# Kernel tuning notes

Measured on AMD Instinct MI355X. Metric: run time of the kernel, lower is better.

Reference implementation:

```python
import math
import jax, jax.numpy as jnp
import numpy as np

CHANNELS = 512
OUT_CHANNELS = 512
N_HEADS = 8
K_CHANNELS = CHANNELS // N_HEADS
WINDOW = 4


def _get_relative_embeddings(emb, length):
    # emb: [1, 2*WINDOW+1, d] -> [1, 2*length-1, d]
    max_rel = 2 * WINDOW + 1
    pad_length = max(0, length - (WINDOW + 1))
    start = max(0, WINDOW + 1 - length)
    end = max_rel + 2 * length - 1
    if pad_length > 0:
        emb = jnp.pad(emb, ((0, 0), (pad_length, pad_length), (0, 0)))
    return emb[:, start:end]


def _rel_to_abs(x):
    # x: [b, h, l, 2l-1] -> [b, h, l, l] via skewing trick
    b, h, l, _ = x.shape
    x = jnp.pad(x, ((0, 0), (0, 0), (0, 0), (0, 1)))
    x_flat = x.reshape(b, h, l * 2 * l)
    x_flat = jnp.pad(x_flat, ((0, 0), (0, 0), (0, l - 1)))
    return x_flat.reshape(b, h, l + 1, 2 * l - 1)[..., :l, l - 1:]


def _abs_to_rel(x):
    # x: [b, h, l, l] -> [b, h, l, 2l-1]
    b, h, l, _ = x.shape
    x = jnp.pad(x, ((0, 0), (0, 0), (0, 0), (0, l - 1)))
    x_flat = x.reshape(b, h, -1)
    x_flat = jnp.pad(x_flat, ((0, 0), (0, 0), (l, 0)))
    return x_flat.reshape(b, h, l, 2 * l)[..., 1:]


def setup_inputs() -> dict:
    key = jax.random.key(0)
    ks = jax.random.split(key, 12)
    B, T = 4, 1024
    w_std = 1.0 / math.sqrt(CHANNELS)
    rel_std = K_CHANNELS ** (-0.5)
    return {
        'x': jax.random.normal(ks[0], (B, T, CHANNELS), jnp.float32),
        'c': jax.random.normal(ks[1], (B, T, CHANNELS), jnp.float32),
        'Wq': jax.random.normal(ks[2], (CHANNELS, CHANNELS), jnp.float32) * w_std,
        'bq': jnp.zeros((CHANNELS,), jnp.float32),
        'Wk': jax.random.normal(ks[3], (CHANNELS, CHANNELS), jnp.float32) * w_std,
        'bk': jnp.zeros((CHANNELS,), jnp.float32),
        'Wv': jax.random.normal(ks[4], (CHANNELS, CHANNELS), jnp.float32) * w_std,
        'bv': jnp.zeros((CHANNELS,), jnp.float32),
        'Wo': jax.random.normal(ks[5], (CHANNELS, OUT_CHANNELS), jnp.float32) * w_std,
        'bo': jnp.zeros((OUT_CHANNELS,), jnp.float32),
        'emb_rel_k': jax.random.normal(ks[6], (1, 2 * WINDOW + 1, K_CHANNELS), jnp.float32) * rel_std,
        'emb_rel_v': jax.random.normal(ks[7], (1, 2 * WINDOW + 1, K_CHANNELS), jnp.float32) * rel_std,
    }


def reference(x, c, Wq, bq, Wk, bk, Wv, bv, Wo, bo, emb_rel_k, emb_rel_v):
    b, t_t, _ = x.shape
    t_s = c.shape[1]
    # 1x1 convs == pointwise dense projections
    q = x @ Wq + bq
    k = c @ Wk + bk
    v = c @ Wv + bv
    q = q.reshape(b, t_t, N_HEADS, K_CHANNELS).transpose(0, 2, 1, 3)
    k = k.reshape(b, t_s, N_HEADS, K_CHANNELS).transpose(0, 2, 1, 3)
    v = v.reshape(b, t_s, N_HEADS, K_CHANNELS).transpose(0, 2, 1, 3)
    q_scaled = q / math.sqrt(K_CHANNELS)
    scores = jnp.einsum('bhtd,bhsd->bhts', q_scaled, k)
    # relative position bias via skewing trick (heads_share=True -> rel emb head dim 1)
    rel_k = _get_relative_embeddings(emb_rel_k, t_s)[0]  # [2*t_s-1, d]
    rel_logits = jnp.einsum('bhtd,md->bhtm', q_scaled, rel_k)
    scores = scores + _rel_to_abs(rel_logits)
    p_attn = jax.nn.softmax(scores, axis=-1)
    out = jnp.einsum('bhts,bhsd->bhtd', p_attn, v)
    rel_w = _abs_to_rel(p_attn)  # [b, h, t, 2t-1]
    rel_v = _get_relative_embeddings(emb_rel_v, t_s)[0]  # [2*t_s-1, d]
    out = out + jnp.einsum('bhtm,md->bhtd', rel_w, rel_v)
    out = out.transpose(0, 2, 1, 3).reshape(b, t_t, CHANNELS)
    return out @ Wo + bo
```

## Files before the change

### kernel.cpp

```cpp
#include <hip/hip_runtime.h>
#include <hip/hip_bf16.h>

#define B_ 4
#define T_ 1024
#define C_ 512
#define H_ 8

typedef __attribute__((ext_vector_type(8))) short short8;
typedef __attribute__((ext_vector_type(4))) float floatx4;

__device__ __forceinline__ unsigned short f2bs(float f) {
    __hip_bfloat16 h = __float2bfloat16(f);
    return *(unsigned short*)&h;
}
__device__ __forceinline__ float bs2f(unsigned short u) {
    __hip_bfloat16 h;
    *(unsigned short*)&h = u;
    return __bfloat162float(h);
}

__device__ __forceinline__ void gload_lds16(const void* g, void* l) {
    __builtin_amdgcn_global_load_lds(
        (const __attribute__((address_space(1))) unsigned int*)g,
        (__attribute__((address_space(3))) unsigned int*)l, 16, 0, 0);
}

__global__ __launch_bounds__(256) void prep(
    const float* __restrict__ x, const float* __restrict__ c,
    const float* __restrict__ Wq, const float* __restrict__ Wk,
    const float* __restrict__ Wv, const float* __restrict__ Wo,
    unsigned short* __restrict__ xb, unsigned short* __restrict__ cb,
    unsigned short* __restrict__ WT)
{
    __shared__ unsigned short tileT[32][33];
    const int bx = blockIdx.x, tid = threadIdx.x;
    if (bx < 2048) {
        const float* src = (bx < 1024) ? x : c;
        unsigned short* dst = (bx < 1024) ? xb : cb;
        const size_t base = (size_t)(bx & 1023) * 2048 + (size_t)tid * 8;
        const float4 a = *(const float4*)&src[base];
        const float4 b = *(const float4*)&src[base + 4];
        short8 o;
        o[0] = (short)f2bs(a.x); o[1] = (short)f2bs(a.y);
        o[2] = (short)f2bs(a.z); o[3] = (short)f2bs(a.w);
        o[4] = (short)f2bs(b.x); o[5] = (short)f2bs(b.y);
        o[6] = (short)f2bs(b.z); o[7] = (short)f2bs(b.w);
        *(short8*)&dst[base] = o;
    } else {
        const int r = bx - 2048;
        const int w = r >> 8, tile = r & 255;
        const int k0 = (tile >> 4) * 32, n0 = (tile & 15) * 32;
        const float* W = (w == 0) ? Wq : (w == 1) ? Wk : (w == 2) ? Wv : Wo;
        unsigned short* out = WT + (size_t)w * 512 * 512;
        const int kk = tid >> 3, ns = (tid & 7) * 4;
        const float4 v = *(const float4*)&W[(size_t)(k0 + kk) * 512 + n0 + ns];
        tileT[ns + 0][kk] = f2bs(v.x);
        tileT[ns + 1][kk] = f2bs(v.y);
        tileT[ns + 2][kk] = f2bs(v.z);
        tileT[ns + 3][kk] = f2bs(v.w);
        __syncthreads();
        const int nn = tid >> 3, ks = (tid & 7) * 4;
        ushort4 o;
        o.x = tileT[nn][ks + 0]; o.y = tileT[nn][ks + 1];
        o.z = tileT[nn][ks + 2]; o.w = tileT[nn][ks + 3];
        *(ushort4*)&out[(size_t)(n0 + nn) * 512 + k0 + ks] = o;
    }
}

template <int BROWS>
__device__ __forceinline__ void gemm_stage(
    const unsigned short* __restrict__ A, const unsigned short* __restrict__ Bt,
    int m0, int n0, int k0, int wave, int lrow, int lseg,
    unsigned short* sAb, unsigned short* sBb)
{
    #pragma unroll
    for (int j = 0; j < 2; j++) {
        const int rA = wave * 32 + j * 16 + lrow;
        gload_lds16((const char*)A + ((size_t)(m0 + rA) * 512 + k0) * 2 + lseg,
                    &sAb[(size_t)(wave * 32 + j * 16) * 32]);
    }
    if constexpr (BROWS == 128) {
        #pragma unroll
        for (int j = 0; j < 2; j++) {
            const int rB = wave * 32 + j * 16 + lrow;
            gload_lds16((const char*)Bt + ((size_t)(n0 + rB) * 512 + k0) * 2 + lseg,
                        &sBb[(size_t)(wave * 32 + j * 16) * 32]);
        }
    } else {
        const int rB = wave * 16 + lrow;
        gload_lds16((const char*)Bt + ((size_t)(n0 + rB) * 512 + k0) * 2 + lseg,
                    &sBb[(size_t)(wave * 16) * 32]);
    }
}

template <int NT>
struct GemmAccT { floatx4 acc[4][NT]; int mrow, kgrp, mhalf, noff; };

template <int NT>
__device__ __forceinline__ void gemm_coreT(
    const unsigned short* __restrict__ A, const unsigned short* __restrict__ Bt,
    int m0, int n0, unsigned short* sA, unsigned short* sB, GemmAccT<NT>& g)
{
    constexpr int BROWS = NT * 32;
    const int tid = threadIdx.x;
    const int wave = tid >> 6, lane = tid & 63;
    g.mrow = lane & 15;
    g.kgrp = (lane >> 4) * 8;
    g.mhalf = (wave & 1) * 64;
    g.noff = (wave >> 1) * (NT * 16);
    const int lrow = lane >> 2;
    const int lseg = (lane & 3) * 16;

    #pragma unroll
    for (int i = 0; i < 4; i++)
        #pragma unroll
        for (int j = 0; j < NT; j++)
            g.acc[i][j] = (floatx4){0.f, 0.f, 0.f, 0.f};

    gemm_stage<BROWS>(A, Bt, m0, n0, 0, wave, lrow, lseg, sA, sB);

    for (int ck = 0; ck < 16; ck++) {
        const int buf = ck & 1;
        __syncthreads();
        if (ck < 15)
            gemm_stage<BROWS>(A, Bt, m0, n0, (ck + 1) * 32, wave, lrow, lseg,
                              sA + (size_t)(buf ^ 1) * 128 * 32,
                              sB + (size_t)(buf ^ 1) * BROWS * 32);
        const unsigned short* sAb = sA + (size_t)buf * 128 * 32;
        const unsigned short* sBb = sB + (size_t)buf * BROWS * 32;
        short8 af[4], bfv[NT];
        #pragma unroll
        for (int i = 0; i < 4; i++)
            af[i] = *(const short8*)&sAb[(size_t)(g.mhalf + i * 16 + g.mrow) * 32 + g.kgrp];
        #pragma unroll
        for (int i = 0; i < NT; i++)
            bfv[i] = *(const short8*)&sBb[(size_t)(g.noff + i * 16 + g.mrow) * 32 + g.kgrp];
        #pragma unroll
        for (int mt = 0; mt < 4; mt++)
            #pragma unroll
            for (int nt = 0; nt < NT; nt++)
                g.acc[mt][nt] = __builtin_amdgcn_mfma_f32_16x16x32_bf16(
                    af[mt], bfv[nt], g.acc[mt][nt], 0, 0, 0);
    }
}

__global__ __launch_bounds__(256) void qkv_mfma(
    const unsigned short* __restrict__ xb, const unsigned short* __restrict__ cb,
    const unsigned short* __restrict__ WT,
    const float* __restrict__ bq, const float* __restrict__ bk,
    const float* __restrict__ bv,
    unsigned short* __restrict__ Qc, unsigned short* __restrict__ Kc,
    unsigned short* __restrict__ Vtg)
{
    const int z = blockIdx.z;
    const unsigned short* A  = (z == 0) ? xb : cb;
    const unsigned short* Bt = WT + (size_t)z * 262144;
    const float* bias        = (z == 0) ? bq : (z == 1) ? bk : bv;
    const float scale        = (z == 0) ? 0.125f : 1.0f;

    __shared__ __align__(16) unsigned short sA[2 * 128 * 32];
    __shared__ __align__(16) unsigned short sB[2 * 128 * 32];

    const int m0 = blockIdx.y * 128, n0 = blockIdx.x * 128;
    GemmAccT<4> g;
    gemm_coreT<4>(A, Bt, m0, n0, sA, sB, g);

    const int lane = threadIdx.x & 63;
    const int rowq = (lane >> 4) * 4;
    if (z < 2) {
        unsigned short* Y = (z == 0) ? Qc : Kc;
        #pragma unroll
        for (int nt = 0; nt < 4; nt++) {
            const int n = n0 + g.noff + nt * 16 + g.mrow;
            const float bv_ = bias[n];
            const int h = n >> 6, d = n & 63;
            #pragma unroll
            for (int mt = 0; mt < 4; mt++)
                #pragma unroll
                for (int r = 0; r < 4; r++) {
                    const int m = m0 + g.mhalf + mt * 16 + rowq + r;
                    const int bb = m >> 10, t = m & 1023;
                    Y[(((size_t)bb * H_ + h) * 1024 + t) * 64 + d] =
                        f2bs((g.acc[mt][nt][r] + bv_) * scale);
                }
        }
    } else {
        #pragma unroll
        for (int nt = 0; nt < 4; nt++) {
            const int n = n0 + g.noff + nt * 16 + g.mrow;
            const float bv_ = bias[n];
            const int h = n >> 6, d = n & 63;
            #pragma unroll
            for (int mt = 0; mt < 4; mt++) {
                const int m = m0 + g.mhalf + mt * 16 + rowq;
                const int bb = m >> 10, t = m & 1023;
                ushort4 o4;
                o4.x = f2bs(g.acc[mt][nt][0] + bv_);
                o4.y = f2bs(g.acc[mt][nt][1] + bv_);
                o4.z = f2bs(g.acc[mt][nt][2] + bv_);
                o4.w = f2bs(g.acc[mt][nt][3] + bv_);
                *(ushort4*)&Vtg[(((size_t)bb * H_ + h) * 64 + d) * 1024 + t] = o4;
            }
        }
    }
}

__global__ __launch_bounds__(256) void out_mfma(
    const unsigned short* __restrict__ AOb, const unsigned short* __restrict__ WoT,
    const float* __restrict__ bias, float* __restrict__ out)
{
    __shared__ __align__(16) unsigned short sA[2 * 128 * 32];
    __shared__ __align__(16) unsigned short sB[2 * 64 * 32];

    const int m0 = blockIdx.y * 128, n0 = blockIdx.x * 64;
    GemmAccT<2> g;
    gemm_coreT<2>(AOb, WoT, m0, n0, sA, sB, g);

    const int lane = threadIdx.x & 63;
    const int rowq = (lane >> 4) * 4;
    #pragma unroll
    for (int nt = 0; nt < 2; nt++) {
        const int n = n0 + g.noff + nt * 16 + g.mrow;
        const float bv_ = bias[n];
        #pragma unroll
        for (int mt = 0; mt < 4; mt++)
            #pragma unroll
            for (int r = 0; r < 4; r++) {
                const int m = m0 + g.mhalf + mt * 16 + rowq + r;
                out[(size_t)m * 512 + n] = g.acc[mt][nt][r] + bv_;
            }
    }
}

__device__ __forceinline__ void attn_stage(
    const unsigned short* __restrict__ Kc, const unsigned short* __restrict__ Vtg,
    size_t qkbase, size_t vtbase, int s0, int wave, int ldrow, int gseg,
    unsigned short* KLb, unsigned short* VtLb)
{
    #pragma unroll
    for (int j = 0; j < 2; j++) {
        const int br = wave * 16 + j * 8;
        gload_lds16((const char*)Kc + (qkbase + (size_t)(s0 + br + ldrow) * 64) * 2 + gseg * 16,
                    &KLb[br * 64]);
        gload_lds16((const char*)Vtg + (vtbase + (size_t)(br + ldrow) * 1024 + s0) * 2 + gseg * 16,
                    &VtLb[br * 64]);
    }
}

__global__ __launch_bounds__(256) void attn_mfma(
    const unsigned short* __restrict__ Qc, const unsigned short* __restrict__ Kc,
    const unsigned short* __restrict__ Vtg,
    const float* __restrict__ rk,
    unsigned short* __restrict__ Opart, float* __restrict__ lpart,
    float* __restrict__ bandP)
{
    __shared__ __align__(16) unsigned short KL[2][64 * 64];
    __shared__ __align__(16) unsigned short VtL[2][64 * 64];
    __shared__ __align__(16) unsigned short PL[4][16 * 72];
    __shared__ float qbL[64 * 9];

    const int tb = blockIdx.x, sh = blockIdx.y, bh = blockIdx.z;
    const int tid = threadIdx.x;
    const int wave = tid >> 6, lane = tid & 63;
    const int t0 = tb * 64;
    const int t0w = t0 + wave * 16;
    const size_t qkbase = (size_t)bh * T_ * 64;
    const size_t vtbase = (size_t)bh * 64 * T_;

    const int mrow = lane & 15;
    const int quad = lane >> 4;
    const int kgrp = quad * 8;
    const int x7 = mrow & 7;
    const int ldrow = lane >> 3;
    const int gseg = (lane & 7) ^ ldrow;

    attn_stage(Kc, Vtg, qkbase, vtbase, sh * 512, wave, ldrow, gseg,
               &KL[0][0], &VtL[0][0]);

    for (int idx = tid; idx < 576; idx += 256) {
        const int row = idx / 9, w = idx - row * 9;
        const unsigned short* qp = &Qc[qkbase + (size_t)(t0 + row) * 64];
        float s = 0.f;
        #pragma unroll
        for (int d8 = 0; d8 < 8; d8++) {
            const short8 q8 = *(const short8*)&qp[d8 * 8];
            #pragma unroll
            for (int i = 0; i < 8; i++)
                s = fmaf(bs2f((unsigned short)q8[i]), rk[w * 64 + d8 * 8 + i], s);
        }
        qbL[idx] = s;
    }

    const short8 aQ0 = *(const short8*)&Qc[qkbase + (size_t)(t0w + mrow) * 64 + kgrp];
    const short8 aQ1 = *(const short8*)&Qc[qkbase + (size_t)(t0w + mrow) * 64 + 32 + kgrp];

    floatx4 Oc[4];
    float ls[4] = {0.f, 0.f, 0.f, 0.f};
    #pragma unroll
    for (int dt = 0; dt < 4; dt++) Oc[dt] = (floatx4){0.f, 0.f, 0.f, 0.f};

    unsigned short* Pw = &PL[wave][0];
    float* qbw = &qbL[wave * 16 * 9];

    for (int ck = 0; ck < 8; ck++) {
        const int s0 = sh * 512 + ck * 64;
        const int buf = ck & 1;
        __syncthreads();
        if (ck < 7)
            attn_stage(Kc, Vtg, qkbase, vtbase, s0 + 64, wave, ldrow, gseg,
                       &KL[buf ^ 1][0], &VtL[buf ^ 1][0]);

        floatx4 Sc[4];
        #pragma unroll
        for (int st = 0; st < 4; st++) {
            const int row = st * 16 + mrow;
            const short8 bK0 = *(const short8*)&KL[buf][row * 64 + (quad ^ x7) * 8];
            const short8 bK1 = *(const short8*)&KL[buf][row * 64 + ((4 + quad) ^ x7) * 8];
            floatx4 s4 = {0.f, 0.f, 0.f, 0.f};
            s4 = __builtin_amdgcn_mfma_f32_16x16x32_bf16(aQ0, bK0, s4, 0, 0, 0);
            s4 = __builtin_amdgcn_mfma_f32_16x16x32_bf16(aQ1, bK1, s4, 0, 0, 0);
            Sc[st] = s4;
        }

        #pragma unroll
        for (int st = 0; st < 4; st++) {
            const int diff = s0 + st * 16 - t0w;
            if (diff >= -19 && diff <= 19) {
                #pragma unroll
                for (int r = 0; r < 4; r++) {
                    const int tloc = quad * 4 + r;
                    const int rel = diff + mrow - tloc;
                    float sc = Sc[st][r];
                    const bool inband = (rel >= -4) && (rel <= 4);
                    if (inband) sc += qbw[tloc * 9 + rel + 4];
                    const float p = __expf(sc);
                    if (inband)
                        bandP[((size_t)bh * 1024 + t0w + tloc) * 9 + rel + 4] = p;
                    Pw[tloc * 72 + st * 16 + mrow] = f2bs(p);
                    ls[r] += p;
                }
            } else {
                #pragma unroll
                for (int r = 0; r < 4; r++) {
                    const int tloc = quad * 4 + r;
                    const float p = __expf(Sc[st][r]);
                    Pw[tloc * 72 + st * 16 + mrow] = f2bs(p);
                    ls[r] += p;
                }
            }
        }

        #pragma unroll
        for (int c = 0; c < 2; c++) {
            const short8 aP = *(const short8*)&Pw[mrow * 72 + c * 32 + kgrp];
            #pragma unroll
            for (int dt = 0; dt < 4; dt++) {
                const int segl = (c * 4 + quad) ^ x7;
                const short8 bV = *(const short8*)&VtL[buf][(dt * 16 + mrow) * 64 + segl * 8];
                Oc[dt] = __builtin_amdgcn_mfma_f32_16x16x32_bf16(aP, bV, Oc[dt], 0, 0, 0);
            }
        }
    }

    float lsum[4];
    #pragma unroll
    for (int r = 0; r < 4; r++) {
        float v = ls[r];
        #pragma unroll
        for (int mk = 1; mk < 16; mk <<= 1)
            v += __shfl_xor(v, mk);
        lsum[r] = v;
    }
    if (mrow == 0) {
        #pragma unroll
        for (int r = 0; r < 4; r++)
            lpart[((size_t)sh * 32 + bh) * 1024 + t0w + quad * 4 + r] = lsum[r];
    }

    const size_t ob = (((size_t)sh * 32 + bh) * 1024 + t0w) * 64;
    #pragma unroll
    for (int dt = 0; dt < 4; dt++)
        #pragma unroll
        for (int r = 0; r < 4; r++)
            Opart[ob + (size_t)(quad * 4 + r) * 64 + dt * 16 + mrow] = f2bs(Oc[dt][r]);
}

__global__ __launch_bounds__(256) void combine(
    const unsigned short* __restrict__ Opart, const float* __restrict__ lpart,
    const float* __restrict__ bandP, const float* __restrict__ rv,
    unsigned short* __restrict__ AOb)
{
    const int bh = blockIdx.y;
    const int b = bh >> 3, h = bh & 7;
    const int tid = threadIdx.x;
    const int tr = tid >> 6, d = tid & 63;
    const int t = blockIdx.x * 4 + tr;

    const size_t i0 = ((size_t)bh * 1024 + t) * 64 + d;
    const size_t half = (size_t)32 * 1024 * 64;
    float o = bs2f(Opart[i0]) + bs2f(Opart[half + i0]);
    const float l = lpart[(size_t)bh * 1024 + t] + lpart[(size_t)32 * 1024 + bh * 1024 + t];
    const float inv = 1.f / l;
    o *= inv;
    #pragma unroll
    for (int w = 0; w < 9; w++) {
        const int s = t + w - 4;
        if (s >= 0 && s < 1024)
            o = fmaf(bandP[((size_t)bh * 1024 + t) * 9 + w] * inv, rv[w * 64 + d], o);
    }
    AOb[((size_t)b * 1024 + t) * 512 + h * 64 + d] = f2bs(o);
}

extern "C" void kernel_launch(void* const* d_in, const int* in_sizes, int n_in,
                              void* d_out, int out_size, void* d_ws, size_t ws_size,
                              hipStream_t stream)
{
    const float* x  = (const float*)d_in[0];
    const float* c  = (const float*)d_in[1];
    const float* Wq = (const float*)d_in[2];
    const float* bq = (const float*)d_in[3];
    const float* Wk = (const float*)d_in[4];
    const float* bk = (const float*)d_in[5];
    const float* Wv = (const float*)d_in[6];
    const float* bv = (const float*)d_in[7];
    const float* Wo = (const float*)d_in[8];
    const float* bo = (const float*)d_in[9];
    const float* rk = (const float*)d_in[10];
    const float* rv = (const float*)d_in[11];

    unsigned short* xb  = (unsigned short*)d_ws;
    unsigned short* cb  = xb + (size_t)4096 * 512;
    unsigned short* WT  = cb + (size_t)4096 * 512;
    unsigned short* Qc  = WT + (size_t)4 * 512 * 512;
    unsigned short* Kc  = Qc + (size_t)32 * 1024 * 64;
    unsigned short* Vtg = Kc + (size_t)32 * 1024 * 64;
    unsigned short* AOb = Vtg + (size_t)32 * 1024 * 64;
    float* lpart = (float*)(AOb + (size_t)4096 * 512);
    float* bandP = lpart + (size_t)2 * 32 * 1024;
    unsigned short* Opart = xb;

    prep<<<3072, 256, 0, stream>>>(x, c, Wq, Wk, Wv, Wo, xb, cb, WT);
    qkv_mfma<<<dim3(4, 32, 3), 256, 0, stream>>>(xb, cb, WT, bq, bk, bv, Qc, Kc, Vtg);
    attn_mfma<<<dim3(16, 2, 32), 256, 0, stream>>>(Qc, Kc, Vtg, rk, Opart, lpart, bandP);
    combine<<<dim3(256, 32), 256, 0, stream>>>(Opart, lpart, bandP, rv, AOb);
    out_mfma<<<dim3(8, 32), 256, 0, stream>>>(AOb, WT + (size_t)3 * 262144, bo, (float*)d_out);
}
```

Baseline: 175.9 us.

## Fuse fp32-to-bf16 conversion into QKV GEMM and merge combine into attention

```diff
diff --git a/kernel.cpp b/kernel.cpp
--- a/kernel.cpp
+++ b/kernel.cpp
@@ -26,126 +26,32 @@
 }
 
 __global__ __launch_bounds__(256) void prep(
-    const float* __restrict__ x, const float* __restrict__ c,
     const float* __restrict__ Wq, const float* __restrict__ Wk,
     const float* __restrict__ Wv, const float* __restrict__ Wo,
-    unsigned short* __restrict__ xb, unsigned short* __restrict__ cb,
     unsigned short* __restrict__ WT)
 {
     __shared__ unsigned short tileT[32][33];
-    const int bx = blockIdx.x, tid = threadIdx.x;
-    if (bx < 2048) {
-        const float* src = (bx < 1024) ? x : c;
-        unsigned short* dst = (bx < 1024) ? xb : cb;
-        const size_t base = (size_t)(bx & 1023) * 2048 + (size_t)tid * 8;
-        const float4 a = *(const float4*)&src[base];
-        const float4 b = *(const float4*)&src[base + 4];
-        short8 o;
-        o[0] = (short)f2bs(a.x); o[1] = (short)f2bs(a.y);
-        o[2] = (short)f2bs(a.z); o[3] = (short)f2bs(a.w);
-        o[4] = (short)f2bs(b.x); o[5] = (short)f2bs(b.y);
-        o[6] = (short)f2bs(b.z); o[7] = (short)f2bs(b.w);
-        *(short8*)&dst[base] = o;
-    } else {
-        const int r = bx - 2048;
-        const int w = r >> 8, tile = r & 255;
-        const int k0 = (tile >> 4) * 32, n0 = (tile & 15) * 32;
-        const float* W = (w == 0) ? Wq : (w == 1) ? Wk : (w == 2) ? Wv : Wo;
-        unsigned short* out = WT + (size_t)w * 512 * 512;
-        const int kk = tid >> 3, ns = (tid & 7) * 4;
-        const float4 v = *(const float4*)&W[(size_t)(k0 + kk) * 512 + n0 + ns];
-        tileT[ns + 0][kk] = f2bs(v.x);
-        tileT[ns + 1][kk] = f2bs(v.y);
-        tileT[ns + 2][kk] = f2bs(v.z);
-        tileT[ns + 3][kk] = f2bs(v.w);
-        __syncthreads();
-        const int nn = tid >> 3, ks = (tid & 7) * 4;
-        ushort4 o;
-        o.x = tileT[nn][ks + 0]; o.y = tileT[nn][ks + 1];
-        o.z = tileT[nn][ks + 2]; o.w = tileT[nn][ks + 3];
-        *(ushort4*)&out[(size_t)(n0 + nn) * 512 + k0 + ks] = o;
-    }
-}
-
-template <int BROWS>
-__device__ __forceinline__ void gemm_stage(
-    const unsigned short* __restrict__ A, const unsigned short* __restrict__ Bt,
-    int m0, int n0, int k0, int wave, int lrow, int lseg,
-    unsigned short* sAb, unsigned short* sBb)
-{
-    #pragma unroll
-    for (int j = 0; j < 2; j++) {
-        const int rA = wave * 32 + j * 16 + lrow;
-        gload_lds16((const char*)A + ((size_t)(m0 + rA) * 512 + k0) * 2 + lseg,
-                    &sAb[(size_t)(wave * 32 + j * 16) * 32]);
-    }
-    if constexpr (BROWS == 128) {
-        #pragma unroll
-        for (int j = 0; j < 2; j++) {
-            const int rB = wave * 32 + j * 16 + lrow;
-            gload_lds16((const char*)Bt + ((size_t)(n0 + rB) * 512 + k0) * 2 + lseg,
-                        &sBb[(size_t)(wave * 32 + j * 16) * 32]);
-        }
-    } else {
-        const int rB = wave * 16 + lrow;
-        gload_lds16((const char*)Bt + ((size_t)(n0 + rB) * 512 + k0) * 2 + lseg,
-                    &sBb[(size_t)(wave * 16) * 32]);
-    }
-}
-
-template <int NT>
-struct GemmAccT { floatx4 acc[4][NT]; int mrow, kgrp, mhalf, noff; };
-
-template <int NT>
-__device__ __forceinline__ void gemm_coreT(
-    const unsigned short* __restrict__ A, const unsigned short* __restrict__ Bt,
-    int m0, int n0, unsigned short* sA, unsigned short* sB, GemmAccT<NT>& g)
-{
-    constexpr int BROWS = NT * 32;
-    const int tid = threadIdx.x;
-    const int wave = tid >> 6, lane = tid & 63;
-    g.mrow = lane & 15;
-    g.kgrp = (lane >> 4) * 8;
-    g.mhalf = (wave & 1) * 64;
-    g.noff = (wave >> 1) * (NT * 16);
-    const int lrow = lane >> 2;
-    const int lseg = (lane & 3) * 16;
-
-    #pragma unroll
-    for (int i = 0; i < 4; i++)
-        #pragma unroll
-        for (int j = 0; j < NT; j++)
-            g.acc[i][j] = (floatx4){0.f, 0.f, 0.f, 0.f};
-
-    gemm_stage<BROWS>(A, Bt, m0, n0, 0, wave, lrow, lseg, sA, sB);
-
-    for (int ck = 0; ck < 16; ck++) {
-        const int buf = ck & 1;
-        __syncthreads();
-        if (ck < 15)
-            gemm_stage<BROWS>(A, Bt, m0, n0, (ck + 1) * 32, wave, lrow, lseg,
-                              sA + (size_t)(buf ^ 1) * 128 * 32,
-                              sB + (size_t)(buf ^ 1) * BROWS * 32);
-        const unsigned short* sAb = sA + (size_t)buf * 128 * 32;
-        const unsigned short* sBb = sB + (size_t)buf * BROWS * 32;
-        short8 af[4], bfv[NT];
-        #pragma unroll
-        for (int i = 0; i < 4; i++)
-            af[i] = *(const short8*)&sAb[(size_t)(g.mhalf + i * 16 + g.mrow) * 32 + g.kgrp];
-        #pragma unroll
-        for (int i = 0; i < NT; i++)
-            bfv[i] = *(const short8*)&sBb[(size_t)(g.noff + i * 16 + g.mrow) * 32 + g.kgrp];
-        #pragma unroll
-        for (int mt = 0; mt < 4; mt++)
-            #pragma unroll
-            for (int nt = 0; nt < NT; nt++)
-                g.acc[mt][nt] = __builtin_amdgcn_mfma_f32_16x16x32_bf16(
-                    af[mt], bfv[nt], g.acc[mt][nt], 0, 0, 0);
-    }
+    const int r = blockIdx.x, tid = threadIdx.x;
+    const int w = r >> 8, tile = r & 255;
+    const int k0 = (tile >> 4) * 32, n0 = (tile & 15) * 32;
+    const float* W = (w == 0) ? Wq : (w == 1) ? Wk : (w == 2) ? Wv : Wo;
+    unsigned short* out = WT + (size_t)w * 512 * 512;
+    const int kk = tid >> 3, ns = (tid & 7) * 4;
+    const float4 v = *(const float4*)&W[(size_t)(k0 + kk) * 512 + n0 + ns];
+    tileT[ns + 0][kk] = f2bs(v.x);
+    tileT[ns + 1][kk] = f2bs(v.y);
+    tileT[ns + 2][kk] = f2bs(v.z);
+    tileT[ns + 3][kk] = f2bs(v.w);
+    __syncthreads();
+    const int nn = tid >> 3, ks = (tid & 7) * 4;
+    ushort4 o;
+    o.x = tileT[nn][ks + 0]; o.y = tileT[nn][ks + 1];
+    o.z = tileT[nn][ks + 2]; o.w = tileT[nn][ks + 3];
+    *(ushort4*)&out[(size_t)(n0 + nn) * 512 + k0 + ks] = o;
 }
 
 __global__ __launch_bounds__(256) void qkv_mfma(
-    const unsigned short* __restrict__ xb, const unsigned short* __restrict__ cb,
+    const float* __restrict__ x, const float* __restrict__ cc,
     const unsigned short* __restrict__ WT,
     const float* __restrict__ bq, const float* __restrict__ bk,
     const float* __restrict__ bv,
@@ -153,52 +59,120 @@
     unsigned short* __restrict__ Vtg)
 {
     const int z = blockIdx.z;
-    const unsigned short* A  = (z == 0) ? xb : cb;
+    const float* A32 = (z == 0) ? x : cc;
     const unsigned short* Bt = WT + (size_t)z * 262144;
-    const float* bias        = (z == 0) ? bq : (z == 1) ? bk : bv;
-    const float scale        = (z == 0) ? 0.125f : 1.0f;
+    const float* bias = (z == 0) ? bq : (z == 1) ? bk : bv;
+    const float scale = (z == 0) ? 0.125f : 1.0f;
 
     __shared__ __align__(16) unsigned short sA[2 * 128 * 32];
-    __shared__ __align__(16) unsigned short sB[2 * 128 * 32];
-
-    const int m0 = blockIdx.y * 128, n0 = blockIdx.x * 128;
-    GemmAccT<4> g;
-    gemm_coreT<4>(A, Bt, m0, n0, sA, sB, g);
-
-    const int lane = threadIdx.x & 63;
-    const int rowq = (lane >> 4) * 4;
+    __shared__ __align__(16) unsigned short sB[2 * 64 * 32];
+
+    const int tid = threadIdx.x;
+    const int wave = tid >> 6, lane = tid & 63;
+    const int m0 = blockIdx.y * 128, n0 = blockIdx.x * 64;
+    const int mrow = lane & 15, quad = lane >> 4, kgrp = quad * 8;
+    const int mhalf = (wave & 1) * 64, noff = (wave >> 1) * 32;
+    const int lrow = lane >> 2, lseg = (lane & 3) * 16;
+
+    const int fr0 = tid >> 3;
+    const int fc4 = (tid & 7) * 4;
+
+    floatx4 acc[4][2];
+    #pragma unroll
+    for (int i = 0; i < 4; i++)
+        #pragma unroll
+        for (int j = 0; j < 2; j++)
+            acc[i][j] = (floatx4){0.f, 0.f, 0.f, 0.f};
+
+    float4 a4[4];
+    #pragma unroll
+    for (int p = 0; p < 4; p++)
+        a4[p] = *(const float4*)&A32[(size_t)(m0 + fr0 + p * 32) * 512 + fc4];
+    {
+        const int rB = wave * 16 + lrow;
+        gload_lds16((const char*)Bt + ((size_t)(n0 + rB) * 512) * 2 + lseg,
+                    &sB[(size_t)(wave * 16) * 32]);
+    }
+    #pragma unroll
+    for (int p = 0; p < 4; p++) {
+        ushort4 o;
+        o.x = f2bs(a4[p].x); o.y = f2bs(a4[p].y);
+        o.z = f2bs(a4[p].z); o.w = f2bs(a4[p].w);
+        *(ushort4*)&sA[(fr0 + p * 32) * 32 + fc4] = o;
+    }
+
+    for (int ck = 0; ck < 16; ck++) {
+        const int buf = ck & 1;
+        __syncthreads();
+        if (ck < 15) {
+            const int k0 = (ck + 1) * 32;
+            const int rB = wave * 16 + lrow;
+            gload_lds16((const char*)Bt + ((size_t)(n0 + rB) * 512 + k0) * 2 + lseg,
+                        &sB[(size_t)((buf ^ 1) * 64 + wave * 16) * 32]);
+            #pragma unroll
+            for (int p = 0; p < 4; p++)
+                a4[p] = *(const float4*)&A32[(size_t)(m0 + fr0 + p * 32) * 512 + k0 + fc4];
+        }
+        const unsigned short* sAb = sA + (size_t)buf * 128 * 32;
+        const unsigned short* sBb = sB + (size_t)buf * 64 * 32;
+        short8 af[4], bfv[2];
+        #pragma unroll
+        for (int i = 0; i < 4; i++)
+            af[i] = *(const short8*)&sAb[(size_t)(mhalf + i * 16 + mrow) * 32 + kgrp];
+        #pragma unroll
+        for (int i = 0; i < 2; i++)
+            bfv[i] = *(const short8*)&sBb[(size_t)(noff + i * 16 + mrow) * 32 + kgrp];
+        #pragma unroll
+        for (int mt = 0; mt < 4; mt++)
+            #pragma unroll
+            for (int nt = 0; nt < 2; nt++)
+                acc[mt][nt] = __builtin_amdgcn_mfma_f32_16x16x32_bf16(
+                    af[mt], bfv[nt], acc[mt][nt], 0, 0, 0);
+        if (ck < 15) {
+            unsigned short* dst = sA + (size_t)(buf ^ 1) * 128 * 32;
+            #pragma unroll
+            for (int p = 0; p < 4; p++) {
+                ushort4 o;
+                o.x = f2bs(a4[p].x); o.y = f2bs(a4[p].y);
+                o.z = f2bs(a4[p].z); o.w = f2bs(a4[p].w);
+                *(ushort4*)&dst[(fr0 + p * 32) * 32 + fc4] = o;
+            }
+        }
+    }
+
+    const int rowq = quad * 4;
     if (z < 2) {
         unsigned short* Y = (z == 0) ? Qc : Kc;
         #pragma unroll
-        for (int nt = 0; nt < 4; nt++) {
-            const int n = n0 + g.noff + nt * 16 + g.mrow;
+        for (int nt = 0; nt < 2; nt++) {
+            const int n = n0 + noff + nt * 16 + mrow;
             const float bv_ = bias[n];
             const int h = n >> 6, d = n & 63;
             #pragma unroll
             for (int mt = 0; mt < 4; mt++)
                 #pragma unroll
                 for (int r = 0; r < 4; r++) {
-                    const int m = m0 + g.mhalf + mt * 16 + rowq + r;
+                    const int m = m0 + mhalf + mt * 16 + rowq + r;
                     const int bb = m >> 10, t = m & 1023;
                     Y[(((size_t)bb * H_ + h) * 1024 + t) * 64 + d] =
-                        f2bs((g.acc[mt][nt][r] + bv_) * scale);
+                        f2bs((acc[mt][nt][r] + bv_) * scale);
                 }
         }
     } else {
         #pragma unroll
-        for (int nt = 0; nt < 4; nt++) {
-            const int n = n0 + g.noff + nt * 16 + g.mrow;
+        for (int nt = 0; nt < 2; nt++) {
+            const int n = n0 + noff + nt * 16 + mrow;
             const float bv_ = bias[n];
             const int h = n >> 6, d = n & 63;
             #pragma unroll
             for (int mt = 0; mt < 4; mt++) {
-                const int m = m0 + g.mhalf + mt * 16 + rowq;
+                const int m = m0 + mhalf + mt * 16 + rowq;
                 const int bb = m >> 10, t = m & 1023;
                 ushort4 o4;
-                o4.x = f2bs(g.acc[mt][nt][0] + bv_);
-                o4.y = f2bs(g.acc[mt][nt][1] + bv_);
-                o4.z = f2bs(g.acc[mt][nt][2] + bv_);
-                o4.w = f2bs(g.acc[mt][nt][3] + bv_);
+                o4.x = f2bs(acc[mt][nt][0] + bv_);
+                o4.y = f2bs(acc[mt][nt][1] + bv_);
+                o4.z = f2bs(acc[mt][nt][2] + bv_);
+                o4.w = f2bs(acc[mt][nt][3] + bv_);
                 *(ushort4*)&Vtg[(((size_t)bb * H_ + h) * 64 + d) * 1024 + t] = o4;
             }
         }
@@ -212,22 +186,65 @@
     __shared__ __align__(16) unsigned short sA[2 * 128 * 32];
     __shared__ __align__(16) unsigned short sB[2 * 64 * 32];
 
+    const int tid = threadIdx.x;
+    const int wave = tid >> 6, lane = tid & 63;
     const int m0 = blockIdx.y * 128, n0 = blockIdx.x * 64;
-    GemmAccT<2> g;
-    gemm_coreT<2>(AOb, WoT, m0, n0, sA, sB, g);
-
-    const int lane = threadIdx.x & 63;
-    const int rowq = (lane >> 4) * 4;
+    const int mrow = lane & 15, quad = lane >> 4, kgrp = quad * 8;
+    const int mhalf = (wave & 1) * 64, noff = (wave >> 1) * 32;
+    const int lrow = lane >> 2, lseg = (lane & 3) * 16;
+
+    floatx4 acc[4][2];
+    #pragma unroll
+    for (int i = 0; i < 4; i++)
+        #pragma unroll
+        for (int j = 0; j < 2; j++)
+            acc[i][j] = (floatx4){0.f, 0.f, 0.f, 0.f};
+
+    auto stage = [&](int k0, int bufi) {
+        #pragma unroll
+        for (int j = 0; j < 2; j++) {
+            const int rA = wave * 32 + j * 16 + lrow;
+            gload_lds16((const char*)AOb + ((size_t)(m0 + rA) * 512 + k0) * 2 + lseg,
+                        &sA[(size_t)(bufi * 128 + wave * 32 + j * 16) * 32]);
+        }
+        const int rB = wave * 16 + lrow;
+        gload_lds16((const char*)WoT + ((size_t)(n0 + rB) * 512 + k0) * 2 + lseg,
+                    &sB[(size_t)(bufi * 64 + wave * 16) * 32]);
+    };
+
+    stage(0, 0);
+    for (int ck = 0; ck < 16; ck++) {
+        const int buf = ck & 1;
+        __syncthreads();
+        if (ck < 15) stage((ck + 1) * 32, buf ^ 1);
+        const unsigned short* sAb = sA + (size_t)buf * 128 * 32;
+        const unsigned short* sBb = sB + (size_t)buf * 64 * 32;
+        short8 af[4], bfv[2];
+        #pragma unroll
+        for (int i = 0; i < 4; i++)
+            af[i] = *(const short8*)&sAb[(size_t)(mhalf + i * 16 + mrow) * 32 + kgrp];
+        #pragma unroll
+        for (int i = 0; i < 2; i++)
+            bfv[i] = *(const short8*)&sBb[(size_t)(noff + i * 16 + mrow) * 32 + kgrp];
+        #pragma unroll
+        for (int mt = 0; mt < 4; mt++)
+            #pragma unroll
+            for (int nt = 0; nt < 2; nt++)
+                acc[mt][nt] = __builtin_amdgcn_mfma_f32_16x16x32_bf16(
+                    af[mt], bfv[nt], acc[mt][nt], 0, 0, 0);
+    }
+
+    const int rowq = quad * 4;
     #pragma unroll
     for (int nt = 0; nt < 2; nt++) {
-        const int n = n0 + g.noff + nt * 16 + g.mrow;
+        const int n = n0 + noff + nt * 16 + mrow;
         const float bv_ = bias[n];
         #pragma unroll
         for (int mt = 0; mt < 4; mt++)
             #pragma unroll
             for (int r = 0; r < 4; r++) {
-                const int m = m0 + g.mhalf + mt * 16 + rowq + r;
-                out[(size_t)m * 512 + n] = g.acc[mt][nt][r] + bv_;
+                const int m = m0 + mhalf + mt * 16 + rowq + r;
+                out[(size_t)m * 512 + n] = acc[mt][nt][r] + bv_;
             }
     }
 }
@@ -250,16 +267,19 @@
 __global__ __launch_bounds__(256) void attn_mfma(
     const unsigned short* __restrict__ Qc, const unsigned short* __restrict__ Kc,
     const unsigned short* __restrict__ Vtg,
-    const float* __restrict__ rk,
-    unsigned short* __restrict__ Opart, float* __restrict__ lpart,
-    float* __restrict__ bandP)
+    const float* __restrict__ rk, const float* __restrict__ rv,
+    unsigned short* __restrict__ AOb)
 {
     __shared__ __align__(16) unsigned short KL[2][64 * 64];
     __shared__ __align__(16) unsigned short VtL[2][64 * 64];
     __shared__ __align__(16) unsigned short PL[4][16 * 72];
     __shared__ float qbL[64 * 9];
-
-    const int tb = blockIdx.x, sh = blockIdx.y, bh = blockIdx.z;
+    __shared__ float bandL[64 * 9];
+    __shared__ float rvL[9 * 64];
+    __shared__ float lL[64];
+
+    const int tb = blockIdx.x, bh = blockIdx.y;
+    const int b = bh >> 3, h = bh & 7;
     const int tid = threadIdx.x;
     const int wave = tid >> 6, lane = tid & 63;
     const int t0 = tb * 64;
@@ -274,39 +294,48 @@
     const int ldrow = lane >> 3;
     const int gseg = (lane & 7) ^ ldrow;
 
-    attn_stage(Kc, Vtg, qkbase, vtbase, sh * 512, wave, ldrow, gseg,
-               &KL[0][0], &VtL[0][0]);
+    attn_stage(Kc, Vtg, qkbase, vtbase, 0, wave, ldrow, gseg, &KL[0][0], &VtL[0][0]);
 
     for (int idx = tid; idx < 576; idx += 256) {
+        bandL[idx] = 0.f;
+        rvL[idx] = rv[idx];
         const int row = idx / 9, w = idx - row * 9;
         const unsigned short* qp = &Qc[qkbase + (size_t)(t0 + row) * 64];
-        float s = 0.f;
-        #pragma unroll
-        for (int d8 = 0; d8 < 8; d8++) {
-            const short8 q8 = *(const short8*)&qp[d8 * 8];
-            #pragma unroll
-            for (int i = 0; i < 8; i++)
-                s = fmaf(bs2f((unsigned short)q8[i]), rk[w * 64 + d8 * 8 + i], s);
-        }
-        qbL[idx] = s;
+        float s0a = 0.f, s1a = 0.f, s2a = 0.f, s3a = 0.f;
+        #pragma unroll
+        for (int d8 = 0; d8 < 8; d8 += 4) {
+            const short8 q0 = *(const short8*)&qp[d8 * 8];
+            const short8 q1 = *(const short8*)&qp[(d8 + 1) * 8];
+            const short8 q2 = *(const short8*)&qp[(d8 + 2) * 8];
+            const short8 q3 = *(const short8*)&qp[(d8 + 3) * 8];
+            #pragma unroll
+            for (int i = 0; i < 8; i++) {
+                s0a = fmaf(bs2f((unsigned short)q0[i]), rk[w * 64 + d8 * 8 + i], s0a);
+                s1a = fmaf(bs2f((unsigned short)q1[i]), rk[w * 64 + (d8 + 1) * 8 + i], s1a);
+                s2a = fmaf(bs2f((unsigned short)q2[i]), rk[w * 64 + (d8 + 2) * 8 + i], s2a);
+                s3a = fmaf(bs2f((unsigned short)q3[i]), rk[w * 64 + (d8 + 3) * 8 + i], s3a);
+            }
+        }
+        qbL[idx] = (s0a + s1a) + (s2a + s3a);
     }
 
     const short8 aQ0 = *(const short8*)&Qc[qkbase + (size_t)(t0w + mrow) * 64 + kgrp];
     const short8 aQ1 = *(const short8*)&Qc[qkbase + (size_t)(t0w + mrow) * 64 + 32 + kgrp];
 
     floatx4 Oc[4];
-    float ls[4] = {0.f, 0.f, 0.f, 0.f};
+    float lsA[4] = {0.f, 0.f, 0.f, 0.f};
     #pragma unroll
     for (int dt = 0; dt < 4; dt++) Oc[dt] = (floatx4){0.f, 0.f, 0.f, 0.f};
 
     unsigned short* Pw = &PL[wave][0];
     float* qbw = &qbL[wave * 16 * 9];
-
-    for (int ck = 0; ck < 8; ck++) {
-        const int s0 = sh * 512 + ck * 64;
+    float* bandw = &bandL[wave * 16 * 9];
+
+    for (int ck = 0; ck < 16; ck++) {
+        const int s0 = ck * 64;
         const int buf = ck & 1;
         __syncthreads();
-        if (ck < 7)
+        if (ck < 15)
             attn_stage(Kc, Vtg, qkbase, vtbase, s0 + 64, wave, ldrow, gseg,
                        &KL[buf ^ 1][0], &VtL[buf ^ 1][0]);
 
@@ -314,40 +343,38 @@
         #pragma unroll
         for (int st = 0; st < 4; st++) {
             const int row = st * 16 + mrow;
-            const short8 bK0 = *(const short8*)&KL[buf][row * 64 + (quad ^ x7) * 8];
-            const short8 bK1 = *(const short8*)&KL[buf][row * 64 + ((4 + quad) ^ x7) * 8];
+            const short8 aK0 = *(const short8*)&KL[buf][row * 64 + (quad ^ x7) * 8];
+            const short8 aK1 = *(const short8*)&KL[buf][row * 64 + ((4 + quad) ^ x7) * 8];
             floatx4 s4 = {0.f, 0.f, 0.f, 0.f};
-            s4 = __builtin_amdgcn_mfma_f32_16x16x32_bf16(aQ0, bK0, s4, 0, 0, 0);
-            s4 = __builtin_amdgcn_mfma_f32_16x16x32_bf16(aQ1, bK1, s4, 0, 0, 0);
+            s4 = __builtin_amdgcn_mfma_f32_16x16x32_bf16(aK0, aQ0, s4, 0, 0, 0);
+            s4 = __builtin_amdgcn_mfma_f32_16x16x32_bf16(aK1, aQ1, s4, 0, 0, 0);
             Sc[st] = s4;
         }
 
         #pragma unroll
         for (int st = 0; st < 4; st++) {
             const int diff = s0 + st * 16 - t0w;
+            float p0, p1, p2, p3;
             if (diff >= -19 && diff <= 19) {
                 #pragma unroll
                 for (int r = 0; r < 4; r++) {
-                    const int tloc = quad * 4 + r;
-                    const int rel = diff + mrow - tloc;
+                    const int rel = diff + quad * 4 + r - mrow;
                     float sc = Sc[st][r];
                     const bool inband = (rel >= -4) && (rel <= 4);
-                    if (inband) sc += qbw[tloc * 9 + rel + 4];
+                    if (inband) sc += qbw[mrow * 9 + rel + 4];
                     const float p = __expf(sc);
-                    if (inband)
-                        bandP[((size_t)bh * 1024 + t0w + tloc) * 9 + rel + 4] = p;
-                    Pw[tloc * 72 + st * 16 + mrow] = f2bs(p);
-                    ls[r] += p;
+                    if (inband) bandw[mrow * 9 + rel + 4] = p;
+                    Sc[st][r] = p;
                 }
             } else {
                 #pragma unroll
-                for (int r = 0; r < 4; r++) {
-                    const int tloc = quad * 4 + r;
-                    const float p = __expf(Sc[st][r]);
-                    Pw[tloc * 72 + st * 16 + mrow] = f2bs(p);
-                    ls[r] += p;
-                }
-            }
+                for (int r = 0; r < 4; r++) Sc[st][r] = __expf(Sc[st][r]);
+            }
+            p0 = Sc[st][0]; p1 = Sc[st][1]; p2 = Sc[st][2]; p3 = Sc[st][3];
+            lsA[st] += (p0 + p1) + (p2 + p3);
+            ushort4 o4;
+            o4.x = f2bs(p0); o4.y = f2bs(p1); o4.z = f2bs(p2); o4.w = f2bs(p3);
+            *(ushort4*)&Pw[mrow * 72 + st * 16 + quad * 4] = o4;
         }
 
         #pragma unroll
@@ -362,53 +389,28 @@
         }
     }
 
-    float lsum[4];
+    float lv = (lsA[0] + lsA[1]) + (lsA[2] + lsA[3]);
+    lv += __shfl_xor(lv, 16);
+    lv += __shfl_xor(lv, 32);
+    if (quad == 0) lL[wave * 16 + mrow] = lv;
+
     #pragma unroll
     for (int r = 0; r < 4; r++) {
-        float v = ls[r];
-        #pragma unroll
-        for (int mk = 1; mk < 16; mk <<= 1)
-            v += __shfl_xor(v, mk);
-        lsum[r] = v;
-    }
-    if (mrow == 0) {
-        #pragma unroll
-        for (int r = 0; r < 4; r++)
-            lpart[((size_t)sh * 32 + bh) * 1024 + t0w + quad * 4 + r] = lsum[r];
-    }
-
-    const size_t ob = (((size_t)sh * 32 + bh) * 1024 + t0w) * 64;
-    #pragma unroll
-    for (int dt = 0; dt < 4; dt++)
-        #pragma unroll
-        for (int r = 0; r < 4; r++)
-            Opart[ob + (size_t)(quad * 4 + r) * 64 + dt * 16 + mrow] = f2bs(Oc[dt][r]);
-}
-
-__global__ __launch_bounds__(256) void combine(
-    const unsigned short* __restrict__ Opart, const float* __restrict__ lpart,
-    const float* __restrict__ bandP, const float* __restrict__ rv,
-    unsigned short* __restrict__ AOb)
-{
-    const int bh = blockIdx.y;
-    const int b = bh >> 3, h = bh & 7;
-    const int tid = threadIdx.x;
-    const int tr = tid >> 6, d = tid & 63;
-    const int t = blockIdx.x * 4 + tr;
-
-    const size_t i0 = ((size_t)bh * 1024 + t) * 64 + d;
-    const size_t half = (size_t)32 * 1024 * 64;
-    float o = bs2f(Opart[i0]) + bs2f(Opart[half + i0]);
-    const float l = lpart[(size_t)bh * 1024 + t] + lpart[(size_t)32 * 1024 + bh * 1024 + t];
-    const float inv = 1.f / l;
-    o *= inv;
-    #pragma unroll
-    for (int w = 0; w < 9; w++) {
-        const int s = t + w - 4;
-        if (s >= 0 && s < 1024)
-            o = fmaf(bandP[((size_t)bh * 1024 + t) * 9 + w] * inv, rv[w * 64 + d], o);
-    }
-    AOb[((size_t)b * 1024 + t) * 512 + h * 64 + d] = f2bs(o);
+        const int tl = quad * 4 + r;
+        const float inv = 1.f / lL[wave * 16 + tl];
+        #pragma unroll
+        for (int w = 0; w < 9; w++) {
+            const float p = bandw[tl * 9 + w];
+            #pragma unroll
+            for (int dt = 0; dt < 4; dt++)
+                Oc[dt][r] = fmaf(p, rvL[w * 64 + dt * 16 + mrow], Oc[dt][r]);
+        }
+        const int t = t0w + tl;
+        #pragma unroll
+        for (int dt = 0; dt < 4; dt++)
+            AOb[((size_t)b * 1024 + t) * 512 + h * 64 + dt * 16 + mrow] =
+                f2bs(Oc[dt][r] * inv);
+    }
 }
 
 extern "C" void kernel_launch(void* const* d_in, const int* in_sizes, int n_in,
@@ -428,20 +430,14 @@
     const float* rk = (const float*)d_in[10];
     const float* rv = (const float*)d_in[11];
 
-    unsigned short* xb  = (unsigned short*)d_ws;
-    unsigned short* cb  = xb + (size_t)4096 * 512;
-    unsigned short* WT  = cb + (size_t)4096 * 512;
+    unsigned short* WT  = (unsigned short*)d_ws;
     unsigned short* Qc  = WT + (size_t)4 * 512 * 512;
     unsigned short* Kc  = Qc + (size_t)32 * 1024 * 64;
     unsigned short* Vtg = Kc + (size_t)32 * 1024 * 64;
     unsigned short* AOb = Vtg + (size_t)32 * 1024 * 64;
-    float* lpart = (float*)(AOb + (size_t)4096 * 512);
-    float* bandP = lpart + (size_t)2 * 32 * 1024;
-    unsigned short* Opart = xb;
-
-    prep<<<3072, 256, 0, stream>>>(x, c, Wq, Wk, Wv, Wo, xb, cb, WT);
-    qkv_mfma<<<dim3(4, 32, 3), 256, 0, stream>>>(xb, cb, WT, bq, bk, bv, Qc, Kc, Vtg);
-    attn_mfma<<<dim3(16, 2, 32), 256, 0, stream>>>(Qc, Kc, Vtg, rk, Opart, lpart, bandP);
-    combine<<<dim3(256, 32), 256, 0, stream>>>(Opart, lpart, bandP, rv, AOb);
+
+    prep<<<1024, 256, 0, stream>>>(Wq, Wk, Wv, Wo, WT);
+    qkv_mfma<<<dim3(8, 32, 3), 256, 0, stream>>>(x, c, WT, bq, bk, bv, Qc, Kc, Vtg);
+    attn_mfma<<<dim3(16, 32), 256, 0, stream>>>(Qc, Kc, Vtg, rk, rv, AOb);
     out_mfma<<<dim3(8, 32), 256, 0, stream>>>(AOb, WT + (size_t)3 * 262144, bo, (float*)d_out);
 }
```

New measurement: 154.9 us. -12.0%, faster.
